# Kernel tuning notes

Measured on AMD Instinct MI355X. Metric: run time of the kernel, lower is better.

## Reference

```python
import jax, jax.numpy as jnp
import numpy as np

B, C, H, W = 4, 256, 32, 32
N_HEADS, N_GROUPS = 8, 4
HEAD_C = C // N_HEADS            # 32
GROUP_C = C // N_GROUPS          # 64
GROUP_HEADS = N_HEADS // N_GROUPS  # 2
OFFSET_RANGE_FACTOR = 4.0
SCALE = HEAD_C ** -0.5
EPS = 1e-5


def grid_sample(img, grid):
    """Bilinear grid_sample, align_corners=True, zeros padding.
    img: (N, Ch, Hi, Wi); grid: (N, Hg, Wg, 2) with (x, y) in [-1, 1]."""
    N, Ch, Hi, Wi = img.shape
    x = (grid[..., 0] + 1.0) * 0.5 * (Wi - 1)
    y = (grid[..., 1] + 1.0) * 0.5 * (Hi - 1)
    x0 = jnp.floor(x); y0 = jnp.floor(y)
    x1 = x0 + 1.0; y1 = y0 + 1.0
    wx1 = x - x0; wx0 = 1.0 - wx1
    wy1 = y - y0; wy0 = 1.0 - wy1
    img_flat = img.reshape(N, Ch, Hi * Wi)

    def corner(xi, yi, w):
        valid = (xi >= 0) & (xi <= Wi - 1) & (yi >= 0) & (yi <= Hi - 1)
        xc = jnp.clip(xi, 0, Wi - 1).astype(jnp.int32)
        yc = jnp.clip(yi, 0, Hi - 1).astype(jnp.int32)
        idx = yc * Wi + xc  # (N, Hg, Wg)
        vals = jax.vmap(lambda im, ix: im[:, ix])(img_flat, idx)  # (N, Ch, Hg, Wg)
        return vals * (w * valid)[:, None, :, :]

    return (corner(x0, y0, wx0 * wy0) + corner(x1, y0, wx1 * wy0)
            + corner(x0, y1, wx0 * wy1) + corner(x1, y1, wx1 * wy1))


def setup_inputs() -> dict:
    key = jax.random.key(0)
    ks = jax.random.split(key, 12)
    s = C ** -0.5
    return {
        "q_feat": jax.random.normal(ks[0], (B, C, H, W), jnp.float32),
        "kv_feat": jax.random.normal(ks[1], (B, C, H, W), jnp.float32),
        "Wq": jax.random.normal(ks[2], (C, C), jnp.float32) * s,
        "bq": jnp.zeros((C,), jnp.float32),
        "Wk": jax.random.normal(ks[3], (C, C), jnp.float32) * s,
        "bk": jnp.zeros((C,), jnp.float32),
        "Wv": jax.random.normal(ks[4], (C, C), jnp.float32) * s,
        "bv": jnp.zeros((C,), jnp.float32),
        "Wo": jax.random.normal(ks[5], (C, C), jnp.float32) * s,
        "bo": jnp.zeros((C,), jnp.float32),
        "off_dw_w": jax.random.normal(ks[6], (GROUP_C, 1, 3, 3), jnp.float32) / 3.0,
        "off_dw_b": jnp.zeros((GROUP_C,), jnp.float32),
        "off_ln_w": jnp.ones((GROUP_C,), jnp.float32),
        "off_ln_b": jnp.zeros((GROUP_C,), jnp.float32),
        "off_pw_w": jax.random.normal(ks[7], (2, GROUP_C), jnp.float32) * GROUP_C ** -0.5,
        "rpe_table": jax.random.normal(ks[8], (N_HEADS, 2 * H - 1, 2 * W - 1), jnp.float32) * 0.01,
    }


def reference(q_feat, kv_feat, Wq, bq, Wk, bk, Wv, bv, Wo, bo,
              off_dw_w, off_dw_b, off_ln_w, off_ln_b, off_pw_w, rpe_table):
    Bg = B * N_GROUPS
    n = H * W
    # q projection (1x1 conv)
    q = jnp.einsum('oi,bihw->bohw', Wq, q_feat) + bq[:, None, None]
    # offset network on grouped q
    q_off = q.reshape(Bg, GROUP_C, H, W)
    x = jax.lax.conv_general_dilated(q_off, off_dw_w, (1, 1), ((1, 1), (1, 1)),
                                     feature_group_count=GROUP_C,
                                     dimension_numbers=('NCHW', 'OIHW', 'NCHW'))
    x = x + off_dw_b[:, None, None]
    mu = x.mean(1, keepdims=True)
    var = x.var(1, keepdims=True)
    x = (x - mu) / jnp.sqrt(var + EPS) * off_ln_w[:, None, None] + off_ln_b[:, None, None]
    x = jax.nn.gelu(x, approximate=False)
    offset = jnp.einsum('oc,bchw->bohw', off_pw_w, x)  # (Bg, 2, H, W), (y, x)
    off_range = jnp.array([1.0 / (H - 1), 1.0 / (W - 1)], jnp.float32).reshape(1, 2, 1, 1)
    offset = jnp.tanh(offset) * off_range * OFFSET_RANGE_FACTOR
    offset = offset.transpose(0, 2, 3, 1)  # (Bg, H, W, 2)
    # reference points in [-1, 1]
    ref_y = (jnp.linspace(0.5, H - 0.5, H) / (H - 1.0)) * 2.0 - 1.0
    ref_x = (jnp.linspace(0.5, W - 0.5, W) / (W - 1.0)) * 2.0 - 1.0
    ref = jnp.stack(jnp.meshgrid(ref_y, ref_x, indexing='ij'), -1)  # (H, W, 2)
    pos = offset + ref[None]  # (Bg, H, W, 2), (y, x), no clamp (offset_range_factor >= 0)
    # deformable sampling of kv features
    kv_g = kv_feat.reshape(Bg, GROUP_C, H, W)
    x_sampled = grid_sample(kv_g, pos[..., ::-1]).reshape(B, C, n)
    k = jnp.einsum('oi,bin->bon', Wk, x_sampled) + bk[:, None]
    v = jnp.einsum('oi,bin->bon', Wv, x_sampled) + bv[:, None]
    qf = q.reshape(B, N_HEADS, HEAD_C, n)
    kf = k.reshape(B, N_HEADS, HEAD_C, n)
    vf = v.reshape(B, N_HEADS, HEAD_C, n)
    attn = jnp.einsum('bhcm,bhcn->bhmn', qf, kf) * SCALE
    # relative-position bias via bilinear sampling of rpe table
    gy = (jnp.arange(H, dtype=jnp.float32) / (H - 1.0)) * 2.0 - 1.0
    gx = (jnp.arange(W, dtype=jnp.float32) / (W - 1.0)) * 2.0 - 1.0
    q_grid = jnp.stack(jnp.meshgrid(gy, gx, indexing='ij'), -1).reshape(n, 2)
    pos_flat = pos.reshape(Bg, n, 2)
    disp = (q_grid[None, :, None, :] - pos_flat[:, None, :, :]) * 0.5  # (Bg, m, n, 2)
    rpe = jnp.broadcast_to(
        rpe_table.reshape(1, N_GROUPS, GROUP_HEADS, 2 * H - 1, 2 * W - 1),
        (B, N_GROUPS, GROUP_HEADS, 2 * H - 1, 2 * W - 1)
    ).reshape(Bg, GROUP_HEADS, 2 * H - 1, 2 * W - 1)
    bias = grid_sample(rpe, disp[..., ::-1])  # (Bg, GROUP_HEADS, m, n)
    attn = attn + bias.reshape(B, N_HEADS, n, n)
    attn = jax.nn.softmax(attn, axis=-1)
    out = jnp.einsum('bhmn,bhcn->bhcm', attn, vf).reshape(B, C, H, W)
    out = jnp.einsum('oi,bihw->bohw', Wo, out) + bo[:, None, None]
    return out
```

## Files before the change

### kernel.cpp

```cpp
#include <hip/hip_runtime.h>
#include <hip/hip_bf16.h>
#include <math.h>
#include <stdint.h>

#define BB 4
#define CC 256
#define HH 32
#define WW 32
#define NPIX 1024
#define NHEADS 8
#define NGROUPS 4
#define HEADC 32
#define GROUPC 64
#define BG 16
#define RPE_N 3969
#define SCALE_QK 0.17677669529663687f
#define LN_EPS 1e-5f

#define W_Q   0
#define W_POS 1048576
#define W_XS  1081344
#define W_KT  2129920
#define W_VV  2654208
#define W_AO  3178496

using frag  = __attribute__((ext_vector_type(8))) short;
using f32x4 = __attribute__((ext_vector_type(4))) float;

struct InPtrs { const void* p[16]; };

__device__ __forceinline__ float tof(float x){ return x; }
__device__ __forceinline__ float tof(__hip_bfloat16 x){ return __bfloat162float(x); }
__device__ __forceinline__ short bfs(float v) {
  __hip_bfloat16 h = __float2bfloat16(v);
  return *(short*)&h;
}
__device__ __forceinline__ bool is_f32(const void* lnw) {
  return *(const unsigned int*)lnw == 0x3F800000u;
}
__device__ __forceinline__ float ldm(const void* p, size_t i, bool f32m) {
  return f32m ? ((const float*)p)[i] : __bfloat162float(((const __hip_bfloat16*)p)[i]);
}
__device__ __forceinline__ float lof(uint32_t g){ return __uint_as_float(g << 16); }
__device__ __forceinline__ float hif(uint32_t g){ return __uint_as_float(g & 0xffff0000u); }

template<int TM>
__device__ __forceinline__ void gemm_body(const void* xsrc, bool xf32,
    const void* wraw, bool wf32, int b, int o0, int mb,
    short* Bs, f32x4* acc) {
  const int tid = threadIdx.x;
  const int wave = tid >> 6, lane = tid & 63, quad = lane >> 4, l15 = lane & 15;
  const int og = wave & 3, mh = wave >> 2;
  const int MS = TM >> 5;
  const int NE = TM >> 4;

  size_t gbase[NE];
  int lbase[NE];
  #pragma unroll
  for (int it = 0; it < NE; ++it) {
    int i = tid + 512 * it;
    int mm = i & (TM - 1), kk = i / TM;
    gbase[it] = ((size_t)(b * CC + kk)) * NPIX + mb + mm;
    lbase[it] = mm * 72 + ((((kk >> 3) ^ (mm & 3))) << 4) + (kk & 7);
  }

  float v[NE];
  #pragma unroll
  for (int it = 0; it < NE; ++it)
    v[it] = xf32 ? ((const float*)xsrc)[gbase[it]]
                 : __bfloat162float(((const __hip_bfloat16*)xsrc)[gbase[it]]);

  for (int s = 0; s < 8; ++s) {
    short* buf = Bs + (s & 1) * (TM * 72);
    #pragma unroll
    for (int it = 0; it < NE; ++it) {
      __hip_bfloat16 h = __float2bfloat16(v[it]);
      buf[lbase[it]] = *(short*)&h;
      buf[lbase[it] + 8] = bfs(v[it] - __bfloat162float(h));
    }
    if (s < 7) {
      size_t koff = (size_t)(s + 1) * 32 * NPIX;
      #pragma unroll
      for (int it = 0; it < NE; ++it)
        v[it] = xf32 ? ((const float*)xsrc)[gbase[it] + koff]
                     : __bfloat162float(((const __hip_bfloat16*)xsrc)[gbase[it] + koff]);
    }
    const int k0 = s * 32;
    size_t wofs = (size_t)(o0 + og * 16 + l15) * CC + k0 + quad * 8;
    float wv[8];
    if (wf32) {
      float4 wa = *(const float4*)((const float*)wraw + wofs);
      float4 wb = *(const float4*)((const float*)wraw + wofs + 4);
      wv[0]=wa.x; wv[1]=wa.y; wv[2]=wa.z; wv[3]=wa.w;
      wv[4]=wb.x; wv[5]=wb.y; wv[6]=wb.z; wv[7]=wb.w;
    } else {
      const __hip_bfloat16* wp = (const __hip_bfloat16*)wraw + wofs;
      #pragma unroll
      for (int j = 0; j < 8; ++j) wv[j] = __bfloat162float(wp[j]);
    }
    frag wh, wl;
    #pragma unroll
    for (int j = 0; j < 8; ++j) {
      __hip_bfloat16 h = __float2bfloat16(wv[j]);
      wh[j] = *(short*)&h;
      wl[j] = bfs(wv[j] - __bfloat162float(h));
    }
    __syncthreads();
    #pragma unroll
    for (int ms = 0; ms < MS; ++ms) {
      int ml = mh * (TM >> 1) + ms * 16 + l15;
      const short* bp = buf + ml * 72 + ((quad ^ (ml & 3)) << 4);
      frag bh = *(const frag*)bp;
      frag bl = *(const frag*)(bp + 8);
      acc[ms] = __builtin_amdgcn_mfma_f32_16x16x32_bf16(wh, bh, acc[ms], 0, 0, 0);
      acc[ms] = __builtin_amdgcn_mfma_f32_16x16x32_bf16(wh, bl, acc[ms], 0, 0, 0);
      acc[ms] = __builtin_amdgcn_mfma_f32_16x16x32_bf16(wl, bh, acc[ms], 0, 0, 0);
    }
  }
}

__global__ __launch_bounds__(512)
void qproj_kernel(InPtrs ip, float* __restrict__ q) {
  __shared__ __align__(16) short Bs[2 * 32 * 72];
  bool f32m = is_f32(ip.p[12]);
  int mb = blockIdx.x * 32, o0 = blockIdx.y * 64, b = blockIdx.z;
  int tid = threadIdx.x;
  int wave = tid >> 6, lane = tid & 63, quad = lane >> 4, l15 = lane & 15;
  f32x4 acc[1] = {{0.f,0.f,0.f,0.f}};
  gemm_body<32>(ip.p[0], f32m, ip.p[2], f32m, b, o0, mb, Bs, acc);
  int og = wave & 3, mh = wave >> 2;
  int od = o0 + og * 16 + quad * 4;
  float bv[4];
  #pragma unroll
  for (int r = 0; r < 4; ++r) bv[r] = ldm(ip.p[3], od + r, f32m);
  int m = mb + mh * 16 + l15;
  #pragma unroll
  for (int r = 0; r < 4; ++r)
    q[(size_t)(b * CC + od + r) * NPIX + m] = acc[0][r] + bv[r];
}

__global__ __launch_bounds__(512)
void kvproj_kernel(InPtrs ip, const float* __restrict__ xs,
                   __hip_bfloat16* __restrict__ kT, __hip_bfloat16* __restrict__ vbf) {
  __shared__ __align__(16) char arena[2 * 64 * 72 * 2];
  bool f32m = is_f32(ip.p[12]);
  int mt = blockIdx.x, ot = blockIdx.y, b = blockIdx.z;
  int mb = mt * 64;
  bool isV = (ot >= 4);
  int o0 = (ot & 3) * 64;
  const void* wraw = isV ? ip.p[6] : ip.p[4];
  const void* braw = isV ? ip.p[7] : ip.p[5];
  int tid = threadIdx.x;
  int wave = tid >> 6, lane = tid & 63, quad = lane >> 4, l15 = lane & 15;
  f32x4 acc[2] = {{0.f,0.f,0.f,0.f},{0.f,0.f,0.f,0.f}};
  gemm_body<64>(xs, true, wraw, f32m, b, o0, mb, (short*)arena, acc);
  int og = wave & 3, mh = wave >> 2;
  int od = o0 + og * 16 + quad * 4;
  float bv[4];
  #pragma unroll
  for (int r = 0; r < 4; ++r) bv[r] = ldm(braw, od + r, f32m);
  if (isV) {
    #pragma unroll
    for (int ms = 0; ms < 2; ++ms) {
      int m = mb + mh * 32 + ms * 16 + l15;
      #pragma unroll
      for (int r = 0; r < 4; ++r)
        vbf[(size_t)(b * CC + od + r) * NPIX + m] = __float2bfloat16(acc[ms][r] + bv[r]);
    }
  } else {
    __syncthreads();
    float* Ds = (float*)arena;
    #pragma unroll
    for (int ms = 0; ms < 2; ++ms) {
      int ml = mh * 32 + ms * 16 + l15;
      #pragma unroll
      for (int r = 0; r < 4; ++r)
        Ds[(og * 16 + quad * 4 + r) * 65 + ml] = acc[ms][r] + bv[r];
    }
    __syncthreads();
    int ot4 = ot & 3;
    {
      int q2 = tid;
      int m = q2 >> 3, cc = q2 & 7;
      __hip_bfloat16 t8[8];
      #pragma unroll
      for (int j = 0; j < 8; ++j)
        t8[j] = __float2bfloat16(Ds[(cc * 8 + j) * 65 + m]);
      int h = ot4 * 2 + (cc >> 2);
      size_t addr = ((size_t)(b * NHEADS + h) * NPIX + mb + m) * HEADC + (cc & 3) * 8;
      *(uint4*)((short*)kT + addr) = *(const uint4*)t8;
    }
  }
}

__global__ __launch_bounds__(512)
void oproj_kernel(InPtrs ip, const float* __restrict__ ao, void* __restrict__ out) {
  __shared__ __align__(16) short Bs[2 * 32 * 72];
  bool f32m = is_f32(ip.p[12]);
  int mb = blockIdx.x * 32, o0 = blockIdx.y * 64, b = blockIdx.z;
  int tid = threadIdx.x;
  int wave = tid >> 6, lane = tid & 63, quad = lane >> 4, l15 = lane & 15;
  f32x4 acc[1] = {{0.f,0.f,0.f,0.f}};
  gemm_body<32>(ao, true, ip.p[8], f32m, b, o0, mb, Bs, acc);
  int og = wave & 3, mh = wave >> 2;
  int od = o0 + og * 16 + quad * 4;
  float bv[4];
  #pragma unroll
  for (int r = 0; r < 4; ++r) bv[r] = ldm(ip.p[9], od + r, f32m);
  int m = mb + mh * 16 + l15;
  #pragma unroll
  for (int r = 0; r < 4; ++r) {
    float val = acc[0][r] + bv[r];
    size_t idx = (size_t)(b * CC + od + r) * NPIX + m;
    if (f32m) ((float*)out)[idx] = val;
    else      ((__hip_bfloat16*)out)[idx] = __float2bfloat16(val);
  }
}

template<typename T>
__device__ __forceinline__ float tap4(const T* __restrict__ img,
                                      int x0, int y0,
                                      float wx0, float wx1, float wy0, float wy1) {
  bool xv0 = (x0 >= 0) & (x0 < WW);
  bool xv1 = (x0 >= -1) & (x0 < WW - 1);
  bool yv0 = (y0 >= 0) & (y0 < HH);
  bool yv1 = (y0 >= -1) & (y0 < HH - 1);
  float acc = 0.0f;
  if (xv0 & yv0) acc += wx0 * wy0 * tof(img[y0 * WW + x0]);
  if (xv1 & yv0) acc += wx1 * wy0 * tof(img[y0 * WW + x0 + 1]);
  if (xv0 & yv1) acc += wx0 * wy1 * tof(img[(y0 + 1) * WW + x0]);
  if (xv1 & yv1) acc += wx1 * wy1 * tof(img[(y0 + 1) * WW + x0 + 1]);
  return acc;
}

__global__ __launch_bounds__(512)
void offsample_kernel(InPtrs ip, const float* __restrict__ q,
                      float* __restrict__ pos, float* __restrict__ xs) {
  __shared__ float qs[128][65];
  __shared__ float posl[2][64];
  bool f32m = is_f32(ip.p[12]);
  int blk = blockIdx.x;
  int hh2 = blk & 15, bg = blk >> 4;
  int b = bg >> 2, g = bg & 3;
  int tid = threadIdx.x;
  const float* qg = q + (size_t)(b * CC + g * GROUPC) * NPIX;
  #pragma unroll
  for (int k = 0; k < 16; ++k) {
    int idx = tid + 512 * k;
    int ww = idx & 31, c = (idx >> 5) & 63, r3 = idx >> 11;
    int yy = hh2 * 2 - 1 + r3;
    float v = (yy >= 0 && yy < HH) ? qg[(size_t)c * NPIX + yy * WW + ww] : 0.0f;
    qs[r3 * 32 + ww][c] = v;
  }
  __syncthreads();
  {
    int wave = tid >> 6, c = tid & 63;
    int lr = wave >> 2, w4 = wave & 3;
    float wdw[9];
    #pragma unroll
    for (int j = 0; j < 9; ++j) wdw[j] = ldm(ip.p[10], c * 9 + j, f32m);
    float bdw = ldm(ip.p[11], c, f32m);
    float lnw = ldm(ip.p[12], c, f32m), lnb = ldm(ip.p[13], c, f32m);
    float pwy = ldm(ip.p[14], c, f32m), pwx = ldm(ip.p[14], GROUPC + c, f32m);

    for (int p8 = 0; p8 < 8; ++p8) {
      int ww = w4 * 8 + p8;
      float x = bdw;
      #pragma unroll
      for (int dy = 0; dy < 3; ++dy)
        #pragma unroll
        for (int dx = 0; dx < 3; ++dx) {
          int xx = ww + dx - 1;
          if (xx >= 0 && xx < WW) x += wdw[dy * 3 + dx] * qs[(lr + dy) * 32 + xx][c];
        }
      float s = x, s2 = x * x;
      #pragma unroll
      for (int off = 32; off > 0; off >>= 1) {
        s  += __shfl_xor(s,  off);
        s2 += __shfl_xor(s2, off);
      }
      float mu  = s * (1.0f / 64.0f);
      float var = s2 * (1.0f / 64.0f) - mu * mu;
      float xn = (x - mu) * (1.0f / sqrtf(var + LN_EPS)) * lnw + lnb;
      float ge = 0.5f * xn * (1.0f + erff(xn * 0.70710678118654752f));
      float oy = pwy * ge, ox = pwx * ge;
      #pragma unroll
      for (int off = 32; off > 0; off >>= 1) {
        oy += __shfl_xor(oy, off);
        ox += __shfl_xor(ox, off);
      }
      if (c == 0) {
        int hh = hh2 * 2 + lr;
        float fy = tanhf(oy) * (4.0f / 31.0f);
        float fx = tanhf(ox) * (4.0f / 31.0f);
        float ry = ((0.5f + (float)hh) / 31.0f) * 2.0f - 1.0f;
        float rx = ((0.5f + (float)ww) / 31.0f) * 2.0f - 1.0f;
        float py = fy + ry, px = fx + rx;
        int m = hh * 32 + ww;
        pos[((size_t)bg * NPIX + m) * 2 + 0] = py;
        pos[((size_t)bg * NPIX + m) * 2 + 1] = px;
        posl[lr][ww * 2 + 0] = py;
        posl[lr][ww * 2 + 1] = px;
      }
    }
  }
  __syncthreads();
  #pragma unroll
  for (int k = 0; k < 8; ++k) {
    int s = tid + 512 * k;
    int ww = s & 31, lr = (s >> 5) & 1, c = s >> 6;
    float py = posl[lr][ww * 2 + 0], px = posl[lr][ww * 2 + 1];
    float xi = (px + 1.0f) * 15.5f, yi = (py + 1.0f) * 15.5f;
    float x0f = floorf(xi), y0f = floorf(yi);
    float wx1 = xi - x0f, wx0 = 1.0f - wx1;
    float wy1 = yi - y0f, wy0 = 1.0f - wy1;
    int x0 = (int)x0f, y0 = (int)y0f;
    size_t img_off = (size_t)(b * CC + g * GROUPC + c) * NPIX;
    float acc;
    if (f32m) acc = tap4((const float*)ip.p[1] + img_off, x0, y0, wx0, wx1, wy0, wy1);
    else      acc = tap4((const __hip_bfloat16*)ip.p[1] + img_off, x0, y0, wx0, wx1, wy0, wy1);
    xs[img_off + (hh2 * 2 + lr) * 32 + ww] = acc;
  }
}

__global__ __launch_bounds__(512, 4)
void attn_mfma_kernel(InPtrs ip, const float* __restrict__ q,
                      const __hip_bfloat16* __restrict__ kT,
                      const __hip_bfloat16* __restrict__ vbf,
                      const float* __restrict__ pos, float* __restrict__ ao) {
  __shared__ __align__(16) __hip_bfloat16 Pl[16][1032];
  __shared__ uint32_t Du[70 * 71];
  __shared__ __align__(16) __hip_bfloat16 qA[4][16][40];
  __shared__ float redmax[8 * 16];
  __shared__ float redsum[8 * 16];

  bool f32m = is_f32(ip.p[12]);
  int bh = blockIdx.x;
  int b = bh >> 3, h = bh & 7;
  int m0base = blockIdx.y * 64;
  int tid = threadIdx.x;
  int bg = b * 4 + (h >> 1);

  size_t slice = (size_t)(b * CC + h * HEADC) * NPIX;
  const short* kTb = (const short*)kT + (size_t)bh * NPIX * HEADC;
  const short* vb = (const short*)vbf + slice;
  const float* qb = q + slice;
  const float* posb = pos + (size_t)bg * NPIX * 2;

  {
    const size_t rbase = (size_t)h * RPE_N;
    for (int i = tid; i < 70 * 71; i += 512) {
      int r = i / 71, c = i - r * 71;
      int y = r - 4, x = c - 4;
      bool yv = (y >= 0) & (y < 63);
      float va = (yv & (x >= 0) & (x < 63)) ? ldm(ip.p[15], rbase + y * 63 + x, f32m) : 0.0f;
      float vb2 = (yv & (x >= -1) & (x < 62)) ? ldm(ip.p[15], rbase + y * 63 + x + 1, f32m) : 0.0f;
      __hip_bfloat16 ha = __float2bfloat16(va), hb = __float2bfloat16(vb2);
      Du[i] = (uint32_t)*(unsigned short*)&ha | ((uint32_t)*(unsigned short*)&hb << 16);
    }
  }
  #pragma unroll
  for (int e = 0; e < 4; ++e) {
    int idx = tid + 512 * e;
    int t = idx >> 9, j = idx & 511;
    int r = j & 15, c = j >> 4;
    qA[t][r][c] = __float2bfloat16(qb[(size_t)c * NPIX + m0base + t * 16 + r] * SCALE_QK);
  }
  __syncthreads();

  int wave = tid >> 6, lane = tid & 63;
  int quad = lane >> 4, l15 = lane & 15;
  int nbase = wave * 128;

  for (int t = 0; t < 4; ++t) {
    int m0 = m0base + t * 16;
    if (t) __syncthreads();

    frag aq = *(const frag*)&qA[t][l15][quad * 8];
    float qgy = (float)(m0 >> 5) * (2.0f / 31.0f) - 1.0f;
    float ybase = 31.0f + 15.5f * qgy;
    float qgx0 = (float)(m0 & 31) * (2.0f / 31.0f) - 1.0f;
    float xbase0 = 31.0f + 15.5f * qgx0;

    float sreg[8][4];
    #pragma unroll
    for (int t8 = 0; t8 < 8; ++t8) {
      int n = nbase + t8 * 16 + l15;
      frag bk = *(const frag*)(kTb + (size_t)n * HEADC + quad * 8);
      f32x4 d = __builtin_amdgcn_mfma_f32_16x16x32_bf16(aq, bk, (f32x4){0.f,0.f,0.f,0.f}, 0, 0, 0);
      float2 pp = *(const float2*)(posb + 2 * n);
      float yi = ybase - 15.5f * pp.x;
      float y0f = floorf(yi);
      float wy1 = yi - y0f, wy0 = 1.0f - wy1;
      float xi0 = xbase0 - 15.5f * pp.y;
      float x0f = floorf(xi0);
      float wx1 = xi0 - x0f, wx0 = 1.0f - wx1;
      int row = (int)y0f + 4;
      int col = (int)x0f + 4 + quad * 4;
      const uint32_t* Dp = Du + row * 71 + col;
      uint32_t g0 = Dp[0],  g1 = Dp[2],  g2 = Dp[4];
      uint32_t h0 = Dp[71], h1 = Dp[73], h2 = Dp[75];
      float u[5];
      u[0] = wy0 * lof(g0) + wy1 * lof(h0);
      u[1] = wy0 * hif(g0) + wy1 * hif(h0);
      u[2] = wy0 * lof(g1) + wy1 * lof(h1);
      u[3] = wy0 * hif(g1) + wy1 * hif(h1);
      u[4] = wy0 * lof(g2) + wy1 * lof(h2);
      #pragma unroll
      for (int reg = 0; reg < 4; ++reg)
        sreg[t8][reg] = d[reg] + wx0 * u[reg] + wx1 * u[reg + 1];
    }

    float ps[4], pm[4];
    #pragma unroll
    for (int reg = 0; reg < 4; ++reg) {
      float m = sreg[0][reg];
      #pragma unroll
      for (int t8 = 1; t8 < 8; ++t8) m = fmaxf(m, sreg[t8][reg]);
      m = fmaxf(m, __shfl_xor(m, 1));
      m = fmaxf(m, __shfl_xor(m, 2));
      m = fmaxf(m, __shfl_xor(m, 4));
      m = fmaxf(m, __shfl_xor(m, 8));
      pm[reg] = m;
      ps[reg] = 0.0f;
    }
    #pragma unroll
    for (int t8 = 0; t8 < 8; ++t8) {
      int n = nbase + t8 * 16 + l15;
      #pragma unroll
      for (int reg = 0; reg < 4; ++reg) {
        float p = __expf(sreg[t8][reg] - pm[reg]);
        Pl[quad * 4 + reg][n] = __float2bfloat16(p);
        ps[reg] += p;
      }
    }
    #pragma unroll
    for (int reg = 0; reg < 4; ++reg) {
      ps[reg] += __shfl_xor(ps[reg], 1);
      ps[reg] += __shfl_xor(ps[reg], 2);
      ps[reg] += __shfl_xor(ps[reg], 4);
      ps[reg] += __shfl_xor(ps[reg], 8);
    }
    if (l15 == 0) {
      #pragma unroll
      for (int reg = 0; reg < 4; ++reg) {
        redmax[wave * 16 + quad * 4 + reg] = pm[reg];
        redsum[wave * 16 + quad * 4 + reg] = ps[reg];
      }
    }

    f32x4 acc0 = {0.f,0.f,0.f,0.f}, acc1 = {0.f,0.f,0.f,0.f};
    #pragma unroll
    for (int ks = 0; ks < 4; ++ks) {
      int koff = nbase + ks * 32 + quad * 8;
      frag ap = *(const frag*)&Pl[l15][koff];
      frag bv0 = *(const frag*)(vb + (size_t)l15 * NPIX + koff);
      frag bv1 = *(const frag*)(vb + (size_t)(16 + l15) * NPIX + koff);
      acc0 = __builtin_amdgcn_mfma_f32_16x16x32_bf16(ap, bv0, acc0, 0, 0, 0);
      acc1 = __builtin_amdgcn_mfma_f32_16x16x32_bf16(ap, bv1, acc1, 0, 0, 0);
    }
    __syncthreads();

    float* part = (float*)&Pl[0][0];
    {
      int e0 = (0 * 16 + l15) * 16 + quad * 4;
      int e1 = (1 * 16 + l15) * 16 + quad * 4;
      #pragma unroll
      for (int reg = 0; reg < 4; ++reg) {
        part[wave * 512 + e0 + reg] = acc0[reg];
        part[wave * 512 + e1 + reg] = acc1[reg];
      }
    }
    __syncthreads();

    {
      int c = tid >> 4, r = tid & 15;
      float M = -1e30f;
      #pragma unroll
      for (int w2 = 0; w2 < 8; ++w2) M = fmaxf(M, redmax[w2 * 16 + r]);
      float num = 0.0f, den = 0.0f;
      #pragma unroll
      for (int w2 = 0; w2 < 8; ++w2) {
        float sc = __expf(redmax[w2 * 16 + r] - M);
        num += part[w2 * 512 + tid] * sc;
        den += redsum[w2 * 16 + r] * sc;
      }
      ao[slice + (size_t)c * NPIX + m0 + r] = num / den;
    }
  }
}

extern "C" void kernel_launch(void* const* d_in, const int* in_sizes, int n_in,
                              void* d_out, int out_size, void* d_ws, size_t ws_size,
                              hipStream_t stream) {
  float* ws  = (float*)d_ws;
  float* q   = ws + W_Q;
  float* pos = ws + W_POS;
  float* xs  = ws + W_XS;
  __hip_bfloat16* kT  = (__hip_bfloat16*)(ws + W_KT);
  __hip_bfloat16* vbf = (__hip_bfloat16*)(ws + W_VV);
  float* ao  = ws + W_AO;

  InPtrs ip;
  for (int i = 0; i < 16; ++i) ip.p[i] = d_in[i];

  qproj_kernel<<<dim3(32, 4, 4), 512, 0, stream>>>(ip, q);
  offsample_kernel<<<BG * 16, 512, 0, stream>>>(ip, q, pos, xs);
  kvproj_kernel<<<dim3(16, 8, 4), 512, 0, stream>>>(ip, xs, kT, vbf);
  attn_mfma_kernel<<<dim3(32, 16), 512, 0, stream>>>(ip, q, kT, vbf, pos, ao);
  oproj_kernel<<<dim3(32, 4, 4), 512, 0, stream>>>(ip, ao, d_out);
}
```

Measured before the change: 185.1 us.

## Split attention row processing into online-softmax halves and shrink shared memory

```diff
diff --git a/kernel.cpp b/kernel.cpp
--- a/kernel.cpp
+++ b/kernel.cpp
@@ -323,14 +323,14 @@
   }
 }
 
-__global__ __launch_bounds__(512, 4)
+__global__ __launch_bounds__(512, 3)
 void attn_mfma_kernel(InPtrs ip, const float* __restrict__ q,
                       const __hip_bfloat16* __restrict__ kT,
                       const __hip_bfloat16* __restrict__ vbf,
                       const float* __restrict__ pos, float* __restrict__ ao) {
   __shared__ __align__(16) __hip_bfloat16 Pl[16][1032];
-  __shared__ uint32_t Du[70 * 71];
-  __shared__ __align__(16) __hip_bfloat16 qA[4][16][40];
+  __shared__ uint32_t Du[68 * 69];
+  __shared__ __align__(16) __hip_bfloat16 qA[16][40];
   __shared__ float redmax[8 * 16];
   __shared__ float redsum[8 * 16];
 
@@ -349,9 +349,9 @@
 
   {
     const size_t rbase = (size_t)h * RPE_N;
-    for (int i = tid; i < 70 * 71; i += 512) {
-      int r = i / 71, c = i - r * 71;
-      int y = r - 4, x = c - 4;
+    for (int i = tid; i < 68 * 69; i += 512) {
+      int r = i / 69, c = i - r * 69;
+      int y = r - 3, x = c - 3;
       bool yv = (y >= 0) & (y < 63);
       float va = (yv & (x >= 0) & (x < 63)) ? ldm(ip.p[15], rbase + y * 63 + x, f32m) : 0.0f;
       float vb2 = (yv & (x >= -1) & (x < 62)) ? ldm(ip.p[15], rbase + y * 63 + x + 1, f32m) : 0.0f;
@@ -359,13 +359,6 @@
       Du[i] = (uint32_t)*(unsigned short*)&ha | ((uint32_t)*(unsigned short*)&hb << 16);
     }
   }
-  #pragma unroll
-  for (int e = 0; e < 4; ++e) {
-    int idx = tid + 512 * e;
-    int t = idx >> 9, j = idx & 511;
-    int r = j & 15, c = j >> 4;
-    qA[t][r][c] = __float2bfloat16(qb[(size_t)c * NPIX + m0base + t * 16 + r] * SCALE_QK);
-  }
   __syncthreads();
 
   int wave = tid >> 6, lane = tid & 63;
@@ -375,65 +368,88 @@
   for (int t = 0; t < 4; ++t) {
     int m0 = m0base + t * 16;
     if (t) __syncthreads();
-
-    frag aq = *(const frag*)&qA[t][l15][quad * 8];
-    float qgy = (float)(m0 >> 5) * (2.0f / 31.0f) - 1.0f;
-    float ybase = 31.0f + 15.5f * qgy;
-    float qgx0 = (float)(m0 & 31) * (2.0f / 31.0f) - 1.0f;
-    float xbase0 = 31.0f + 15.5f * qgx0;
-
-    float sreg[8][4];
-    #pragma unroll
-    for (int t8 = 0; t8 < 8; ++t8) {
-      int n = nbase + t8 * 16 + l15;
-      frag bk = *(const frag*)(kTb + (size_t)n * HEADC + quad * 8);
-      f32x4 d = __builtin_amdgcn_mfma_f32_16x16x32_bf16(aq, bk, (f32x4){0.f,0.f,0.f,0.f}, 0, 0, 0);
-      float2 pp = *(const float2*)(posb + 2 * n);
-      float yi = ybase - 15.5f * pp.x;
-      float y0f = floorf(yi);
-      float wy1 = yi - y0f, wy0 = 1.0f - wy1;
-      float xi0 = xbase0 - 15.5f * pp.y;
-      float x0f = floorf(xi0);
-      float wx1 = xi0 - x0f, wx0 = 1.0f - wx1;
-      int row = (int)y0f + 4;
-      int col = (int)x0f + 4 + quad * 4;
-      const uint32_t* Dp = Du + row * 71 + col;
-      uint32_t g0 = Dp[0],  g1 = Dp[2],  g2 = Dp[4];
-      uint32_t h0 = Dp[71], h1 = Dp[73], h2 = Dp[75];
-      float u[5];
-      u[0] = wy0 * lof(g0) + wy1 * lof(h0);
-      u[1] = wy0 * hif(g0) + wy1 * hif(h0);
-      u[2] = wy0 * lof(g1) + wy1 * lof(h1);
-      u[3] = wy0 * hif(g1) + wy1 * hif(h1);
-      u[4] = wy0 * lof(g2) + wy1 * lof(h2);
-      #pragma unroll
-      for (int reg = 0; reg < 4; ++reg)
-        sreg[t8][reg] = d[reg] + wx0 * u[reg] + wx1 * u[reg + 1];
-    }
-
-    float ps[4], pm[4];
-    #pragma unroll
-    for (int reg = 0; reg < 4; ++reg) {
-      float m = sreg[0][reg];
-      #pragma unroll
-      for (int t8 = 1; t8 < 8; ++t8) m = fmaxf(m, sreg[t8][reg]);
-      m = fmaxf(m, __shfl_xor(m, 1));
-      m = fmaxf(m, __shfl_xor(m, 2));
-      m = fmaxf(m, __shfl_xor(m, 4));
-      m = fmaxf(m, __shfl_xor(m, 8));
-      pm[reg] = m;
-      ps[reg] = 0.0f;
-    }
-    #pragma unroll
-    for (int t8 = 0; t8 < 8; ++t8) {
-      int n = nbase + t8 * 16 + l15;
+    {
+      int r = tid & 15, c = tid >> 4;
+      qA[r][c] = __float2bfloat16(qb[(size_t)c * NPIX + m0 + r] * SCALE_QK);
+    }
+    __syncthreads();
+
+    frag aq = *(const frag*)&qA[l15][quad * 8];
+    float ybase = 31.0f + 15.5f * ((float)(m0 >> 5) * (2.0f / 31.0f) - 1.0f);
+    float xbase0 = 31.0f + 15.5f * ((float)(m0 & 31) * (2.0f / 31.0f) - 1.0f);
+
+    float pm[4], ps[4];
+    f32x4 acc0 = {0.f,0.f,0.f,0.f}, acc1 = {0.f,0.f,0.f,0.f};
+    #pragma unroll
+    for (int reg = 0; reg < 4; ++reg) { pm[reg] = -1e30f; ps[reg] = 0.0f; }
+
+    #pragma unroll
+    for (int half = 0; half < 2; ++half) {
+      int hbase = nbase + half * 64;
+      float sreg[4][4];
+      #pragma unroll
+      for (int t8 = 0; t8 < 4; ++t8) {
+        int n = hbase + t8 * 16 + l15;
+        frag bk = *(const frag*)(kTb + (size_t)n * HEADC + quad * 8);
+        f32x4 d = __builtin_amdgcn_mfma_f32_16x16x32_bf16(aq, bk, (f32x4){0.f,0.f,0.f,0.f}, 0, 0, 0);
+        float2 pp = *(const float2*)(posb + 2 * n);
+        float yi = ybase - 15.5f * pp.x;
+        float y0f = floorf(yi);
+        float wy1 = yi - y0f, wy0 = 1.0f - wy1;
+        float xi0 = xbase0 - 15.5f * pp.y;
+        float x0f = floorf(xi0);
+        float wx1 = xi0 - x0f, wx0 = 1.0f - wx1;
+        int row = (int)y0f + 3;
+        int col = (int)x0f + 3 + quad * 4;
+        const uint32_t* Dp = Du + row * 69 + col;
+        uint32_t g0 = Dp[0],  g1 = Dp[2],  g2 = Dp[4];
+        uint32_t h0 = Dp[69], h1 = Dp[71], h2 = Dp[73];
+        float u[5];
+        u[0] = wy0 * lof(g0) + wy1 * lof(h0);
+        u[1] = wy0 * hif(g0) + wy1 * hif(h0);
+        u[2] = wy0 * lof(g1) + wy1 * lof(h1);
+        u[3] = wy0 * hif(g1) + wy1 * hif(h1);
+        u[4] = wy0 * lof(g2) + wy1 * lof(h2);
+        #pragma unroll
+        for (int reg = 0; reg < 4; ++reg)
+          sreg[t8][reg] = d[reg] + wx0 * u[reg] + wx1 * u[reg + 1];
+      }
       #pragma unroll
       for (int reg = 0; reg < 4; ++reg) {
-        float p = __expf(sreg[t8][reg] - pm[reg]);
-        Pl[quad * 4 + reg][n] = __float2bfloat16(p);
-        ps[reg] += p;
-      }
-    }
+        float m = fmaxf(fmaxf(sreg[0][reg], sreg[1][reg]),
+                        fmaxf(sreg[2][reg], sreg[3][reg]));
+        m = fmaxf(m, __shfl_xor(m, 1));
+        m = fmaxf(m, __shfl_xor(m, 2));
+        m = fmaxf(m, __shfl_xor(m, 4));
+        m = fmaxf(m, __shfl_xor(m, 8));
+        float newm = fmaxf(pm[reg], m);
+        float sc = __expf(pm[reg] - newm);
+        pm[reg] = newm;
+        ps[reg] *= sc;
+        acc0[reg] *= sc;
+        acc1[reg] *= sc;
+      }
+      #pragma unroll
+      for (int t8 = 0; t8 < 4; ++t8) {
+        int n = hbase + t8 * 16 + l15;
+        #pragma unroll
+        for (int reg = 0; reg < 4; ++reg) {
+          float p = __expf(sreg[t8][reg] - pm[reg]);
+          Pl[quad * 4 + reg][n] = __float2bfloat16(p);
+          ps[reg] += p;
+        }
+      }
+      #pragma unroll
+      for (int ks = 0; ks < 2; ++ks) {
+        int koff = hbase + ks * 32 + quad * 8;
+        frag ap = *(const frag*)&Pl[l15][koff];
+        frag bv0 = *(const frag*)(vb + (size_t)l15 * NPIX + koff);
+        frag bv1 = *(const frag*)(vb + (size_t)(16 + l15) * NPIX + koff);
+        acc0 = __builtin_amdgcn_mfma_f32_16x16x32_bf16(ap, bv0, acc0, 0, 0, 0);
+        acc1 = __builtin_amdgcn_mfma_f32_16x16x32_bf16(ap, bv1, acc1, 0, 0, 0);
+      }
+    }
+
     #pragma unroll
     for (int reg = 0; reg < 4; ++reg) {
       ps[reg] += __shfl_xor(ps[reg], 1);
@@ -447,17 +463,6 @@
         redmax[wave * 16 + quad * 4 + reg] = pm[reg];
         redsum[wave * 16 + quad * 4 + reg] = ps[reg];
       }
-    }
-
-    f32x4 acc0 = {0.f,0.f,0.f,0.f}, acc1 = {0.f,0.f,0.f,0.f};
-    #pragma unroll
-    for (int ks = 0; ks < 4; ++ks) {
-      int koff = nbase + ks * 32 + quad * 8;
-      frag ap = *(const frag*)&Pl[l15][koff];
-      frag bv0 = *(const frag*)(vb + (size_t)l15 * NPIX + koff);
-      frag bv1 = *(const frag*)(vb + (size_t)(16 + l15) * NPIX + koff);
-      acc0 = __builtin_amdgcn_mfma_f32_16x16x32_bf16(ap, bv0, acc0, 0, 0, 0);
-      acc1 = __builtin_amdgcn_mfma_f32_16x16x32_bf16(ap, bv1, acc1, 0, 0, 0);
     }
     __syncthreads();
 
```

After: 194.0 us. 1.05x slower.
